# Optimization experiments

Hardware: AMD Instinct MI355X
Metric: run time of the kernel (lower is better)

Reference implementation:

```python
import jax, jax.numpy as jnp
import numpy as np

TEMPERATURE = 0.07
EPS = 1e-12  # F.normalize eps


def setup_inputs() -> dict:
    key = jax.random.key(0)
    k1, k2, k3 = jax.random.split(key, 3)
    B, D, N_CLASSES = 4096, 256, 1000
    return {
        "z_i": jax.random.normal(k1, (B, D), dtype=jnp.float32),
        "z_j": jax.random.normal(k2, (B, D), dtype=jnp.float32),
        "labels": jax.random.randint(k3, (B,), 0, N_CLASSES, dtype=jnp.int64),
    }


def _l2_normalize(x):
    norm = jnp.sqrt(jnp.sum(x * x, axis=1, keepdims=True))
    return x / jnp.maximum(norm, EPS)


def reference(z_i, z_j, labels):
    zi = _l2_normalize(z_i)
    zj = _l2_normalize(z_j)
    z = jnp.concatenate([zi, zj], axis=0)          # (2B, D)
    lab = jnp.concatenate([labels, labels], axis=0)  # (2B,)
    N = z.shape[0]

    sim = jnp.matmul(z, z.T) / TEMPERATURE          # (2B, 2B)

    eye = jnp.eye(N, dtype=bool)
    same = lab[:, None] == lab[None, :]
    pos_mask = same & ~eye                          # positives: same label, not self
    neg_mask = ~same                                # negatives: different label

    # pos_sim_i = sum of similarities over positives (a sum, per original code)
    pos_sim = jnp.sum(jnp.where(pos_mask, sim, 0.0), axis=1)  # (2B,)
    # log(neg_sim_i) = logsumexp over negatives (stable, same math as sum of exp)
    lse_neg = jax.nn.logsumexp(jnp.where(neg_mask, sim, -jnp.inf), axis=1)
    # -log(exp(p) / (exp(p) + n)) = log(1 + exp(log n - p))
    loss_i = jnp.logaddexp(0.0, lse_neg - pos_sim)  # (2B,)

    has_pos = jnp.any(pos_mask, axis=1)
    loss = jnp.sum(jnp.where(has_pos, loss_i, 0.0)) / N
    return loss
```

## Files before the change

kernel.cpp:

```cpp
#include <hip/hip_runtime.h>

#define NROWS 8192
#define BQ    4096
#define DDIM  256
#define INV_T (1.0f/0.07f)
#define K2EXP (1.4426950408889634f/0.07f)

typedef short bf16x8 __attribute__((ext_vector_type(8)));
typedef float f32x4  __attribute__((ext_vector_type(4)));
typedef unsigned short u16;

__device__ __forceinline__ u16 f2bf(float f) {
  unsigned u = __float_as_uint(f);
  u += 0x7fffu + ((u >> 16) & 1u);
  return (u16)(u >> 16);
}

__global__ void norm_cast_kernel(const float* __restrict__ zi,
                                 const float* __restrict__ zj,
                                 u16* __restrict__ zb) {
  int wave = threadIdx.x >> 6;
  int lane = threadIdx.x & 63;
  int row  = blockIdx.x * 4 + wave;
  const float* src = (row < BQ) ? (zi + (size_t)row * DDIM)
                                : (zj + (size_t)(row - BQ) * DDIM);
  float4 v = ((const float4*)src)[lane];
  float s = v.x*v.x + v.y*v.y + v.z*v.z + v.w*v.w;
  #pragma unroll
  for (int m = 32; m; m >>= 1) s += __shfl_xor(s, m, 64);
  float scale = 1.0f / fmaxf(sqrtf(s), 1e-12f);
  ushort4 o;
  o.x = f2bf(v.x * scale); o.y = f2bf(v.y * scale);
  o.z = f2bf(v.z * scale); o.w = f2bf(v.w * scale);
  ((ushort4*)(zb + (size_t)row * DDIM))[lane] = o;
}

#define GL2LDS(gp, lp) \
  __builtin_amdgcn_global_load_lds((__attribute__((address_space(1))) void*)(gp), \
                                   (__attribute__((address_space(3))) void*)(lp), 16, 0, 0)

__global__ __launch_bounds__(256) void simloss_kernel(
    const u16* __restrict__ zb, const int* __restrict__ labels,
    float* __restrict__ pos_p, float* __restrict__ neg_p) {
  __shared__ __align__(16) u16 lsA[128 * 32];
  __shared__ __align__(16) u16 lsB[128 * 32];

  const int tid  = threadIdx.x;
  const int w    = tid >> 6;
  const int lane = tid & 63;
  const int ln   = lane & 15;
  const int qd   = lane >> 4;
  const int wr   = w >> 1;
  const int wc   = w & 1;
  const int r0   = blockIdx.x * 128;
  const int cb   = blockIdx.y * 1024;

  const int strow = lane >> 2;
  const int slot  = lane & 3;
  const int stk   = (slot ^ ((strow >> 1) & 3)) * 8;
  const int rdsw  = (ln >> 1) & 3;

  int rowidx[16], rowlab[16];
  #pragma unroll
  for (int ri = 0; ri < 4; ++ri)
    #pragma unroll
    for (int r = 0; r < 4; ++r) {
      int slt = ri * 4 + r;
      int row = r0 + wr * 64 + ri * 16 + qd * 4 + r;
      rowidx[slt] = row;
      rowlab[slt] = labels[row & (BQ - 1)];
    }

  float posA[16], negA[16];
  #pragma unroll
  for (int i = 0; i < 16; ++i) { posA[i] = 0.0f; negA[i] = 0.0f; }

  for (int ci = 0; ci < 8; ++ci) {
    const int c0 = cb + ci * 128;
    int colv[4], clab[4];
    #pragma unroll
    for (int mi = 0; mi < 4; ++mi) {
      colv[mi] = c0 + wc * 64 + mi * 16 + ln;
      clab[mi] = labels[colv[mi] & (BQ - 1)];
    }

    const f32x4 z4 = {0.f, 0.f, 0.f, 0.f};
    f32x4 acc[4][4];
    #pragma unroll
    for (int ri = 0; ri < 4; ++ri)
      #pragma unroll
      for (int mi = 0; mi < 4; ++mi) acc[ri][mi] = z4;

    for (int kk = 0; kk < 8; ++kk) {
      const int k0 = kk * 32;
      #pragma unroll
      for (int j = 0; j < 2; ++j) {
        int rbase = w * 32 + j * 16;
        const u16* ga = zb + (size_t)(r0 + rbase + strow) * DDIM + k0 + stk;
        GL2LDS(ga, &lsA[rbase * 32]);
        const u16* gb = zb + (size_t)(c0 + rbase + strow) * DDIM + k0 + stk;
        GL2LDS(gb, &lsB[rbase * 32]);
      }
      __syncthreads();

      bf16x8 av[4], bv[4];
      #pragma unroll
      for (int ri = 0; ri < 4; ++ri)
        av[ri] = *(const bf16x8*)&lsA[(wr * 64 + ri * 16 + ln) * 32 + (qd ^ rdsw) * 8];
      #pragma unroll
      for (int mi = 0; mi < 4; ++mi)
        bv[mi] = *(const bf16x8*)&lsB[(wc * 64 + mi * 16 + ln) * 32 + (qd ^ rdsw) * 8];
      #pragma unroll
      for (int ri = 0; ri < 4; ++ri)
        #pragma unroll
        for (int mi = 0; mi < 4; ++mi)
          acc[ri][mi] = __builtin_amdgcn_mfma_f32_16x16x32_bf16(
              av[ri], bv[mi], acc[ri][mi], 0, 0, 0);
      __syncthreads();
    }

    #pragma unroll
    for (int ri = 0; ri < 4; ++ri)
      #pragma unroll
      for (int mi = 0; mi < 4; ++mi) {
        f32x4 v = acc[ri][mi];
        #pragma unroll
        for (int r = 0; r < 4; ++r) {
          int slt = ri * 4 + r;
          float s = v[r];
          bool same = (rowlab[slt] == clab[mi]);
          bool diag = (rowidx[slt] == colv[mi]);
          posA[slt] += (same && !diag) ? s : 0.0f;
          negA[slt] += same ? 0.0f : __builtin_amdgcn_exp2f(s * K2EXP);
        }
      }
  }

  #pragma unroll
  for (int i = 0; i < 16; ++i) {
    #pragma unroll
    for (int m = 1; m < 16; m <<= 1) {
      posA[i] += __shfl_xor(posA[i], m, 64);
      negA[i] += __shfl_xor(negA[i], m, 64);
    }
  }
  if (ln == 0) {
    int s = blockIdx.y * 2 + wc;
    #pragma unroll
    for (int i = 0; i < 16; ++i) {
      pos_p[(size_t)s * NROWS + rowidx[i]] = posA[i];
      neg_p[(size_t)s * NROWS + rowidx[i]] = negA[i];
    }
  }
}

__global__ void loss_kernel(const float* __restrict__ pos_p,
                            const float* __restrict__ neg_p,
                            float* __restrict__ out) {
  int row = blockIdx.x * 256 + threadIdx.x;
  float p = 0.0f, n = 0.0f;
  #pragma unroll
  for (int s = 0; s < 16; ++s) {
    p += pos_p[(size_t)s * NROWS + row];
    n += neg_p[(size_t)s * NROWS + row];
  }
  float l = log1pf(expf(logf(n) - p * INV_T));
  #pragma unroll
  for (int m = 32; m; m >>= 1) l += __shfl_xor(l, m, 64);
  __shared__ float red[4];
  if ((threadIdx.x & 63) == 0) red[threadIdx.x >> 6] = l;
  __syncthreads();
  if (threadIdx.x == 0) {
    float tot = red[0] + red[1] + red[2] + red[3];
    atomicAdd(out, tot * (1.0f / NROWS));
  }
}

extern "C" void kernel_launch(void* const* d_in, const int* in_sizes, int n_in,
                              void* d_out, int out_size, void* d_ws, size_t ws_size,
                              hipStream_t stream) {
  const float* zi     = (const float*)d_in[0];
  const float* zj     = (const float*)d_in[1];
  const int*   labels = (const int*)d_in[2];
  float*       out    = (float*)d_out;

  char* w = (char*)d_ws;
  u16*   zb    = (u16*)w;
  float* pos_p = (float*)(w + (size_t)NROWS * DDIM * sizeof(u16));
  float* neg_p = pos_p + 16 * NROWS;

  hipMemsetAsync(out, 0, sizeof(float), stream);
  hipLaunchKernelGGL(norm_cast_kernel, dim3(2048), dim3(256), 0, stream, zi, zj, zb);
  hipLaunchKernelGGL(simloss_kernel, dim3(64, 8), dim3(256), 0, stream,
                     zb, labels, pos_p, neg_p);
  hipLaunchKernelGGL(loss_kernel, dim3(32), dim3(256), 0, stream,
                     pos_p, neg_p, out);
}
```

Baseline: 121.5 us.

## Keep full A row tile resident in LDS and stream B fragments from global

The similarity kernel now loads its whole 128x256 bf16 row tile into LDS once (64 KB, XOR-swizzled) instead of re-staging A and B per k-step. B fragments are read directly from global memory into registers with a three-deep rotation, and A fragments are double-buffered from LDS, which removes the per-k __syncthreads. The diagonal check is skipped for off-diagonal tiles, and the output memset is folded into the normalize kernel. In exchange, the kernel uses much more LDS per block and relies on direct global loads for B, which may cost latency and limit occupancy.

```diff
diff --git a/kernel.cpp b/kernel.cpp
--- a/kernel.cpp
+++ b/kernel.cpp
@@ -18,7 +18,9 @@
 
 __global__ void norm_cast_kernel(const float* __restrict__ zi,
                                  const float* __restrict__ zj,
-                                 u16* __restrict__ zb) {
+                                 u16* __restrict__ zb,
+                                 float* __restrict__ out) {
+  if (blockIdx.x == 0 && threadIdx.x == 0) *out = 0.0f;
   int wave = threadIdx.x >> 6;
   int lane = threadIdx.x & 63;
   int row  = blockIdx.x * 4 + wave;
@@ -39,11 +41,10 @@
   __builtin_amdgcn_global_load_lds((__attribute__((address_space(1))) void*)(gp), \
                                    (__attribute__((address_space(3))) void*)(lp), 16, 0, 0)
 
-__global__ __launch_bounds__(256) void simloss_kernel(
+__global__ __launch_bounds__(256, 2) void simloss_kernel(
     const u16* __restrict__ zb, const int* __restrict__ labels,
     float* __restrict__ pos_p, float* __restrict__ neg_p) {
-  __shared__ __align__(16) u16 lsA[128 * 32];
-  __shared__ __align__(16) u16 lsB[128 * 32];
+  __shared__ __align__(16) u16 lsA[128 * 256];
 
   const int tid  = threadIdx.x;
   const int w    = tid >> 6;
@@ -55,33 +56,43 @@
   const int r0   = blockIdx.x * 128;
   const int cb   = blockIdx.y * 1024;
 
-  const int strow = lane >> 2;
-  const int slot  = lane & 3;
-  const int stk   = (slot ^ ((strow >> 1) & 3)) * 8;
-  const int rdsw  = (ln >> 1) & 3;
-
-  int rowidx[16], rowlab[16];
+  #pragma unroll
+  for (int j = 0; j < 16; ++j) {
+    int base = w * 32 + j * 2;
+    int row  = base + (lane >> 5);
+    int gcol = ((lane & 31) ^ (row & 7)) * 8;
+    GL2LDS(zb + (size_t)(r0 + row) * DDIM + gcol, &lsA[base * 256]);
+  }
+
+  int rowlab[16];
   #pragma unroll
   for (int ri = 0; ri < 4; ++ri)
     #pragma unroll
     for (int r = 0; r < 4; ++r) {
-      int slt = ri * 4 + r;
       int row = r0 + wr * 64 + ri * 16 + qd * 4 + r;
-      rowidx[slt] = row;
-      rowlab[slt] = labels[row & (BQ - 1)];
+      rowlab[ri * 4 + r] = labels[row & (BQ - 1)];
     }
 
   float posA[16], negA[16];
   #pragma unroll
   for (int i = 0; i < 16; ++i) { posA[i] = 0.0f; negA[i] = 0.0f; }
+
+  const int axor = ln & 7;
+  int arow[4];
+  #pragma unroll
+  for (int ri = 0; ri < 4; ++ri) arow[ri] = (wr * 64 + ri * 16 + ln) * DDIM;
+
+  __syncthreads();
 
   for (int ci = 0; ci < 8; ++ci) {
     const int c0 = cb + ci * 128;
     int colv[4], clab[4];
+    const u16* bp[4];
     #pragma unroll
     for (int mi = 0; mi < 4; ++mi) {
       colv[mi] = c0 + wc * 64 + mi * 16 + ln;
       clab[mi] = labels[colv[mi] & (BQ - 1)];
+      bp[mi]   = zb + (size_t)colv[mi] * DDIM + qd * 8;
     }
 
     const f32x4 z4 = {0.f, 0.f, 0.f, 0.f};
@@ -91,49 +102,68 @@
       #pragma unroll
       for (int mi = 0; mi < 4; ++mi) acc[ri][mi] = z4;
 
+    bf16x8 av[2][4], bv[3][4];
+    #pragma unroll
+    for (int ri = 0; ri < 4; ++ri)
+      av[0][ri] = *(const bf16x8*)&lsA[arow[ri] + (qd ^ axor) * 8];
+    #pragma unroll
+    for (int mi = 0; mi < 4; ++mi) bv[0][mi] = *(const bf16x8*)(bp[mi]);
+    #pragma unroll
+    for (int mi = 0; mi < 4; ++mi) bv[1][mi] = *(const bf16x8*)(bp[mi] + 32);
+
+    #pragma unroll
     for (int kk = 0; kk < 8; ++kk) {
-      const int k0 = kk * 32;
-      #pragma unroll
-      for (int j = 0; j < 2; ++j) {
-        int rbase = w * 32 + j * 16;
-        const u16* ga = zb + (size_t)(r0 + rbase + strow) * DDIM + k0 + stk;
-        GL2LDS(ga, &lsA[rbase * 32]);
-        const u16* gb = zb + (size_t)(c0 + rbase + strow) * DDIM + k0 + stk;
-        GL2LDS(gb, &lsB[rbase * 32]);
+      if (kk < 7) {
+        #pragma unroll
+        for (int ri = 0; ri < 4; ++ri)
+          av[(kk + 1) & 1][ri] = *(const bf16x8*)
+              &lsA[arow[ri] + ((((kk + 1) * 4 + qd) ^ axor)) * 8];
       }
-      __syncthreads();
-
-      bf16x8 av[4], bv[4];
-      #pragma unroll
-      for (int ri = 0; ri < 4; ++ri)
-        av[ri] = *(const bf16x8*)&lsA[(wr * 64 + ri * 16 + ln) * 32 + (qd ^ rdsw) * 8];
-      #pragma unroll
-      for (int mi = 0; mi < 4; ++mi)
-        bv[mi] = *(const bf16x8*)&lsB[(wc * 64 + mi * 16 + ln) * 32 + (qd ^ rdsw) * 8];
+      if (kk < 6) {
+        #pragma unroll
+        for (int mi = 0; mi < 4; ++mi)
+          bv[(kk + 2) % 3][mi] = *(const bf16x8*)(bp[mi] + (kk + 2) * 32);
+      }
       #pragma unroll
       for (int ri = 0; ri < 4; ++ri)
         #pragma unroll
         for (int mi = 0; mi < 4; ++mi)
           acc[ri][mi] = __builtin_amdgcn_mfma_f32_16x16x32_bf16(
-              av[ri], bv[mi], acc[ri][mi], 0, 0, 0);
-      __syncthreads();
-    }
-
-    #pragma unroll
-    for (int ri = 0; ri < 4; ++ri)
-      #pragma unroll
-      for (int mi = 0; mi < 4; ++mi) {
-        f32x4 v = acc[ri][mi];
-        #pragma unroll
-        for (int r = 0; r < 4; ++r) {
-          int slt = ri * 4 + r;
-          float s = v[r];
-          bool same = (rowlab[slt] == clab[mi]);
-          bool diag = (rowidx[slt] == colv[mi]);
-          posA[slt] += (same && !diag) ? s : 0.0f;
-          negA[slt] += same ? 0.0f : __builtin_amdgcn_exp2f(s * K2EXP);
+              av[kk & 1][ri], bv[kk % 3][mi], acc[ri][mi], 0, 0, 0);
+    }
+
+    if (r0 == c0) {
+      #pragma unroll
+      for (int ri = 0; ri < 4; ++ri)
+        #pragma unroll
+        for (int mi = 0; mi < 4; ++mi) {
+          f32x4 v = acc[ri][mi];
+          #pragma unroll
+          for (int r = 0; r < 4; ++r) {
+            int slt = ri * 4 + r;
+            float s = v[r];
+            bool same = (rowlab[slt] == clab[mi]);
+            bool diag = ((r0 + wr * 64 + ri * 16 + qd * 4 + r) == colv[mi]);
+            posA[slt] += (same && !diag) ? s : 0.0f;
+            negA[slt] += same ? 0.0f : __builtin_amdgcn_exp2f(s * K2EXP);
+          }
         }
-      }
+    } else {
+      #pragma unroll
+      for (int ri = 0; ri < 4; ++ri)
+        #pragma unroll
+        for (int mi = 0; mi < 4; ++mi) {
+          f32x4 v = acc[ri][mi];
+          #pragma unroll
+          for (int r = 0; r < 4; ++r) {
+            int slt = ri * 4 + r;
+            float s = v[r];
+            bool same = (rowlab[slt] == clab[mi]);
+            posA[slt] += same ? s : 0.0f;
+            negA[slt] += same ? 0.0f : __builtin_amdgcn_exp2f(s * K2EXP);
+          }
+        }
+    }
   }
 
   #pragma unroll
@@ -148,8 +178,9 @@
     int s = blockIdx.y * 2 + wc;
     #pragma unroll
     for (int i = 0; i < 16; ++i) {
-      pos_p[(size_t)s * NROWS + rowidx[i]] = posA[i];
-      neg_p[(size_t)s * NROWS + rowidx[i]] = negA[i];
+      int row = r0 + wr * 64 + (i >> 2) * 16 + qd * 4 + (i & 3);
+      pos_p[(size_t)s * NROWS + row] = posA[i];
+      neg_p[(size_t)s * NROWS + row] = negA[i];
     }
   }
 }
@@ -189,8 +220,8 @@
   float* pos_p = (float*)(w + (size_t)NROWS * DDIM * sizeof(u16));
   float* neg_p = pos_p + 16 * NROWS;
 
-  hipMemsetAsync(out, 0, sizeof(float), stream);
-  hipLaunchKernelGGL(norm_cast_kernel, dim3(2048), dim3(256), 0, stream, zi, zj, zb);
+  hipLaunchKernelGGL(norm_cast_kernel, dim3(2048), dim3(256), 0, stream,
+                     zi, zj, zb, out);
   hipLaunchKernelGGL(simloss_kernel, dim3(64, 8), dim3(256), 0, stream,
                      zb, labels, pos_p, neg_p);
   hipLaunchKernelGGL(loss_kernel, dim3(32), dim3(256), 0, stream,
```

Measured after the change: 165.4 us. 1.36x slower.
